# Kernel tuning notes

Measured on AMD Instinct MI355X. Metric: run time of the kernel, lower is better.

The kernel has to match this reference:

```python
import jax, jax.numpy as jnp
import numpy as np

N = 100000   # nodes
E = 1600000  # edges
DIN = 128
HID = 128
D2 = 64      # hard-coded last-conv width in the module
OUT = 1000


def setup_inputs() -> dict:
    key = jax.random.key(0)
    ks = jax.random.split(key, 8)
    x = jax.random.normal(ks[0], (N, DIN), dtype=jnp.float32)
    edge_index = jax.random.randint(ks[1], (2, E), 0, N, dtype=jnp.int64)
    W1 = jax.random.normal(ks[2], (DIN, HID), dtype=jnp.float32) * 0.05
    b1 = jnp.zeros((HID,), dtype=jnp.float32)
    W2 = jax.random.normal(ks[3], (HID, D2), dtype=jnp.float32) * 0.05
    b2 = jnp.zeros((D2,), dtype=jnp.float32)
    Wfc = jax.random.normal(ks[4], (D2, OUT), dtype=jnp.float32) * 0.05
    bfc = jnp.zeros((OUT,), dtype=jnp.float32)
    return {"x": x, "W1": W1, "b1": b1, "W2": W2, "b2": b2,
            "Wfc": Wfc, "bfc": bfc, "edge_index": edge_index}


def _gcn_conv(x, W, b, src, dst):
    # PyG GCNConv: h = X W; add self-loops; symmetric norm D^-1/2 (A+I) D^-1/2; + bias
    h = x @ W                                   # [N, F]
    ones = jnp.ones(src.shape[0], dtype=h.dtype)
    deg = jax.ops.segment_sum(ones, dst, num_segments=N) + 1.0  # +1 for self-loop
    dinv = jax.lax.rsqrt(deg)                   # [N]
    norm = dinv[src] * dinv[dst]                # [E]
    agg = jax.ops.segment_sum(h[src] * norm[:, None], dst, num_segments=N)
    agg = agg + h * (dinv * dinv)[:, None]      # self-loop contribution
    return agg + b


def reference(x, W1, b1, W2, b2, Wfc, bfc, edge_index):
    src, dst = edge_index[0], edge_index[1]
    h = jax.nn.relu(_gcn_conv(x, W1, b1, src, dst))
    # dropout is identity in eval mode (training=False)
    h = jax.nn.relu(_gcn_conv(h, W2, b2, src, dst))
    return h @ Wfc + bfc
```

## Files before the change

kernel.cpp:

```cpp
#include <hip/hip_runtime.h>
#include <hip/hip_bf16.h>
#include <cstddef>

typedef __attribute__((ext_vector_type(8))) short bf16x8;
typedef __attribute__((ext_vector_type(4))) float f32x4;

__device__ __forceinline__ unsigned short f2bf(float f) {
    __hip_bfloat16 h = __float2bfloat16(f);
    return __builtin_bit_cast(unsigned short, h);
}
__device__ __forceinline__ float bf2f(unsigned short u) {
    return __bfloat162float(__builtin_bit_cast(__hip_bfloat16, u));
}
__device__ __forceinline__ float bflo(unsigned u) {
    return __builtin_bit_cast(float, u << 16);
}
__device__ __forceinline__ float bfhi(unsigned u) {
    return __builtin_bit_cast(float, u & 0xffff0000u);
}


__global__ void k_zero_i(int* __restrict__ p, int total) {
    int i = blockIdx.x * blockDim.x + threadIdx.x;
    int stride = gridDim.x * blockDim.x;
    for (; i < total; i += stride) p[i] = 0;
}


__global__ void k_deg_i(const int* __restrict__ dst, int* __restrict__ deg, int E) {
    int e = blockIdx.x * blockDim.x + threadIdx.x;
    if (e < E) atomicAdd(&deg[dst[e]], 1);
}


#define SCAN_B 1024

__global__ void k_scan1(const int* __restrict__ in, int* __restrict__ out,
                        int* __restrict__ sums, float* __restrict__ dinv, int n) {
    __shared__ int tmp[SCAN_B];
    int tid = threadIdx.x;
    int gid = blockIdx.x * SCAN_B + tid;
    int v = (gid < n) ? in[gid] : 0;
    if (gid < n) dinv[gid] = rsqrtf((float)v + 1.0f);
    tmp[tid] = v;
    __syncthreads();
    for (int off = 1; off < SCAN_B; off <<= 1) {
        int t = (tid >= off) ? tmp[tid - off] : 0;
        __syncthreads();
        tmp[tid] += t;
        __syncthreads();
    }
    if (gid < n) out[gid] = tmp[tid] - v;
    if (tid == SCAN_B - 1) sums[blockIdx.x] = tmp[tid];
}

__global__ void k_scan2(int* __restrict__ sums, int nb) {
    __shared__ int tmp[128];
    int tid = threadIdx.x;
    int v = (tid < nb) ? sums[tid] : 0;
    tmp[tid] = v;
    __syncthreads();
    for (int off = 1; off < 128; off <<= 1) {
        int t = (tid >= off) ? tmp[tid - off] : 0;
        __syncthreads();
        tmp[tid] += t;
        __syncthreads();
    }
    if (tid < nb) sums[tid] = tmp[tid] - v;
}

__global__ void k_scan3(int* __restrict__ out, int* __restrict__ cursor,
                        const int* __restrict__ sums, int n) {
    int gid = blockIdx.x * SCAN_B + threadIdx.x;
    if (gid < n) {
        int v = out[gid] + sums[blockIdx.x];
        out[gid] = v;
        cursor[gid] = v;
    }
}


__global__ void k_fill(const int* __restrict__ src, const int* __restrict__ dst,
                       int* __restrict__ cursor, int* __restrict__ csr_src, int E) {
    int e = blockIdx.x * blockDim.x + threadIdx.x;
    if (e < E) {
        int pos = atomicAdd(&cursor[dst[e]], 1);
        csr_src[pos] = src[e];
    }
}


__global__ void k_conv_w_bf(const float* __restrict__ W, unsigned short* __restrict__ Bh,
                            int K, int N)
{
    int n = blockIdx.x;
    int k = threadIdx.x;
    Bh[(size_t)n * K + k] = f2bf(W[(size_t)k * N + n]);
}

__global__ void k_conv_w(const float* __restrict__ W, unsigned short* __restrict__ Bh,
                         unsigned short* __restrict__ Bl, int K, int N)
{
    int n = blockIdx.x;
    int k = threadIdx.x;
    float v = W[(size_t)k * N + n];
    unsigned short hi = f2bf(v);
    unsigned short lo = f2bf(v - bf2f(hi));
    Bh[(size_t)n * K + k] = hi;
    Bl[(size_t)n * K + k] = lo;
}


__device__ __forceinline__ void unpack_fma(float* a, float w, uint4 v) {
    a[0] = fmaf(w, bflo(v.x), a[0]);
    a[1] = fmaf(w, bfhi(v.x), a[1]);
    a[2] = fmaf(w, bflo(v.y), a[2]);
    a[3] = fmaf(w, bfhi(v.y), a[3]);
    a[4] = fmaf(w, bflo(v.z), a[4]);
    a[5] = fmaf(w, bfhi(v.z), a[5]);
    a[6] = fmaf(w, bflo(v.w), a[6]);
    a[7] = fmaf(w, bfhi(v.w), a[7]);
}

__launch_bounds__(256)
__global__ void k_gather128(const unsigned short* __restrict__ hbf,
                            const int* __restrict__ csr_src, const int* __restrict__ off,
                            const float* __restrict__ dinv, const float* __restrict__ bias,
                            unsigned short* __restrict__ obf, int N, int E)
{
    int node = blockIdx.x * 4 + (threadIdx.x >> 6);
    int lane = threadIdx.x & 63;
    if (node >= N) return;
    float dn = dinv[node];
    int beg = off[node];
    int end = (node + 1 < N) ? off[node + 1] : E;

    const int grp = lane >> 4;
    const int sub = lane & 15;

    uint4 sv = make_uint4(0, 0, 0, 0);
    float4 b0 = make_float4(0.f, 0.f, 0.f, 0.f), b1 = b0;
    if (grp == 0) {
        sv = *(const uint4*)(hbf + (size_t)node * 128 + sub * 8);
        b0 = *(const float4*)(bias + sub * 8);
        b1 = *(const float4*)(bias + sub * 8 + 4);
    }

    float a[8] = {0.f, 0.f, 0.f, 0.f, 0.f, 0.f, 0.f, 0.f};
    int i = beg + grp;
    for (; i + 12 < end; i += 16) {
        int s0 = csr_src[i];
        int s1 = csr_src[i + 4];
        int s2 = csr_src[i + 8];
        int s3 = csr_src[i + 12];
        float w0 = dinv[s0] * dn;
        float w1 = dinv[s1] * dn;
        float w2 = dinv[s2] * dn;
        float w3 = dinv[s3] * dn;
        uint4 v0 = *(const uint4*)(hbf + (size_t)s0 * 128 + sub * 8);
        uint4 v1 = *(const uint4*)(hbf + (size_t)s1 * 128 + sub * 8);
        uint4 v2 = *(const uint4*)(hbf + (size_t)s2 * 128 + sub * 8);
        uint4 v3 = *(const uint4*)(hbf + (size_t)s3 * 128 + sub * 8);
        unpack_fma(a, w0, v0);
        unpack_fma(a, w1, v1);
        unpack_fma(a, w2, v2);
        unpack_fma(a, w3, v3);
    }
    for (; i < end; i += 4) {
        int s = csr_src[i];
        float w = dinv[s] * dn;
        uint4 v = *(const uint4*)(hbf + (size_t)s * 128 + sub * 8);
        unpack_fma(a, w, v);
    }

#pragma unroll
    for (int k = 0; k < 8; ++k) {
        a[k] += __shfl_xor(a[k], 16);
        a[k] += __shfl_xor(a[k], 32);
    }

    if (grp == 0) {
        float s[8] = {bflo(sv.x), bfhi(sv.x), bflo(sv.y), bfhi(sv.y),
                      bflo(sv.z), bfhi(sv.z), bflo(sv.w), bfhi(sv.w)};
        float bv[8] = {b0.x, b0.y, b0.z, b0.w, b1.x, b1.y, b1.z, b1.w};
        float w = dn * dn;
        unsigned short o[8];
#pragma unroll
        for (int k = 0; k < 8; ++k)
            o[k] = f2bf(fmaxf(fmaf(s[k], w, a[k]) + bv[k], 0.f));
        uint4 vo;
        vo.x = (unsigned)o[0] | ((unsigned)o[1] << 16);
        vo.y = (unsigned)o[2] | ((unsigned)o[3] << 16);
        vo.z = (unsigned)o[4] | ((unsigned)o[5] << 16);
        vo.w = (unsigned)o[6] | ((unsigned)o[7] << 16);
        *(uint4*)(obf + (size_t)node * 128 + sub * 8) = vo;
    }
}


__launch_bounds__(256)
__global__ void k_gather64(const unsigned short* __restrict__ hbf,
                           const int* __restrict__ csr_src, const int* __restrict__ off,
                           const float* __restrict__ dinv, const float* __restrict__ bias,
                           unsigned short* __restrict__ hhi, unsigned short* __restrict__ hlo,
                           int N, int E)
{
    int node = blockIdx.x * 4 + (threadIdx.x >> 6);
    int lane = threadIdx.x & 63;
    if (node >= N) return;
    float dn = dinv[node];
    int beg = off[node];
    int end = (node + 1 < N) ? off[node + 1] : E;

    const int grp = lane >> 3;
    const int sub = lane & 7;

    uint4 sv = make_uint4(0, 0, 0, 0);
    float4 b0 = make_float4(0.f, 0.f, 0.f, 0.f), b1 = b0;
    if (grp == 0) {
        sv = *(const uint4*)(hbf + (size_t)node * 64 + sub * 8);
        b0 = *(const float4*)(bias + sub * 8);
        b1 = *(const float4*)(bias + sub * 8 + 4);
    }

    float a[8] = {0.f, 0.f, 0.f, 0.f, 0.f, 0.f, 0.f, 0.f};
    int i = beg + grp;
    for (; i + 8 < end; i += 16) {
        int s0 = csr_src[i];
        int s1 = csr_src[i + 8];
        float w0 = dinv[s0] * dn;
        float w1 = dinv[s1] * dn;
        uint4 v0 = *(const uint4*)(hbf + (size_t)s0 * 64 + sub * 8);
        uint4 v1 = *(const uint4*)(hbf + (size_t)s1 * 64 + sub * 8);
        unpack_fma(a, w0, v0);
        unpack_fma(a, w1, v1);
    }
    if (i < end) {
        int s = csr_src[i];
        float w = dinv[s] * dn;
        uint4 v = *(const uint4*)(hbf + (size_t)s * 64 + sub * 8);
        unpack_fma(a, w, v);
    }

#pragma unroll
    for (int k = 0; k < 8; ++k) {
        a[k] += __shfl_xor(a[k], 8);
        a[k] += __shfl_xor(a[k], 16);
        a[k] += __shfl_xor(a[k], 32);
    }

    if (grp == 0) {
        float s[8] = {bflo(sv.x), bfhi(sv.x), bflo(sv.y), bfhi(sv.y),
                      bflo(sv.z), bfhi(sv.z), bflo(sv.w), bfhi(sv.w)};
        float bv[8] = {b0.x, b0.y, b0.z, b0.w, b1.x, b1.y, b1.z, b1.w};
        float w = dn * dn;
        unsigned short hi[8], lo[8];
#pragma unroll
        for (int k = 0; k < 8; ++k) {
            float f = fmaxf(fmaf(s[k], w, a[k]) + bv[k], 0.f);
            hi[k] = f2bf(f);
            lo[k] = f2bf(f - bf2f(hi[k]));
        }
        uint4 vh, vl;
        vh.x = (unsigned)hi[0] | ((unsigned)hi[1] << 16);
        vh.y = (unsigned)hi[2] | ((unsigned)hi[3] << 16);
        vh.z = (unsigned)hi[4] | ((unsigned)hi[5] << 16);
        vh.w = (unsigned)hi[6] | ((unsigned)hi[7] << 16);
        vl.x = (unsigned)lo[0] | ((unsigned)lo[1] << 16);
        vl.y = (unsigned)lo[2] | ((unsigned)lo[3] << 16);
        vl.z = (unsigned)lo[4] | ((unsigned)lo[5] << 16);
        vl.w = (unsigned)lo[6] | ((unsigned)lo[7] << 16);
        *(uint4*)(hhi + (size_t)node * 64 + sub * 8) = vh;
        *(uint4*)(hlo + (size_t)node * 64 + sub * 8) = vl;
    }
}


__launch_bounds__(256, 2)
__global__ void gemm_mfma_l1(const float* __restrict__ A,
                             const unsigned short* __restrict__ Bt,
                             unsigned short* __restrict__ Cbf, int M)
{
    __shared__ unsigned short Ah[128 * 64];
    __shared__ unsigned short Bh[128 * 64];

    const int tid = threadIdx.x;
    const int m0 = blockIdx.x * 128;
    const int lane = tid & 63, wave = tid >> 6;
    const int wr = wave >> 1, wc = wave & 1;
    const int lrow = lane & 15, kgrp = lane >> 4;

    f32x4 acc[4][4] = {};

    for (int ph = 0; ph < 2; ++ph) {
        const int k0 = ph * 64;
        __syncthreads();
        {
            const int c4 = tid & 15, r0 = tid >> 4;
#pragma unroll
            for (int p = 0; p < 8; ++p) {
                int row = r0 + p * 16;
                int gr = m0 + row; if (gr >= M) gr = M - 1;
                float4 v = *(const float4*)(A + (size_t)gr * 128 + k0 + c4 * 4);
                ushort4 hv;
                hv.x = f2bf(v.x); hv.y = f2bf(v.y); hv.z = f2bf(v.z); hv.w = f2bf(v.w);
                *(ushort4*)((char*)Ah + row * 128 + ((c4 * 8) ^ ((row & 7) << 4))) = hv;
            }
        }
        {
            const int c = tid & 7, col0 = tid >> 3;
#pragma unroll
            for (int p = 0; p < 4; ++p) {
                int col = col0 + p * 32;
                uint4 v = *(const uint4*)(Bt + (size_t)col * 128 + k0 + c * 8);
                *(uint4*)((char*)Bh + col * 128 + ((c * 16) ^ ((col & 7) << 4))) = v;
            }
        }
        __syncthreads();

#pragma unroll
        for (int ks = 0; ks < 2; ++ks) {
            const int cIdx = kgrp + ks * 4;
            bf16x8 ah[4], bh[4];
#pragma unroll
            for (int i = 0; i < 4; ++i) {
                int row = wr * 64 + i * 16 + lrow;
                ah[i] = *(const bf16x8*)((const char*)Ah + row * 128 + ((cIdx * 16) ^ ((row & 7) << 4)));
            }
#pragma unroll
            for (int j = 0; j < 4; ++j) {
                int col = wc * 64 + j * 16 + lrow;
                bh[j] = *(const bf16x8*)((const char*)Bh + col * 128 + ((cIdx * 16) ^ ((col & 7) << 4)));
            }
#pragma unroll
            for (int i = 0; i < 4; ++i)
#pragma unroll
                for (int j = 0; j < 4; ++j)
                    acc[i][j] = __builtin_amdgcn_mfma_f32_16x16x32_bf16(bh[j], ah[i], acc[i][j], 0, 0, 0);
        }
    }

#pragma unroll
    for (int i = 0; i < 4; ++i) {
        int grow = m0 + wr * 64 + i * 16 + lrow;
        if (grow >= M) continue;
        unsigned short* crow = Cbf + (size_t)grow * 128;
#pragma unroll
        for (int j = 0; j < 4; ++j) {
            int gc = wc * 64 + j * 16 + kgrp * 4;
            ushort4 o;
            o.x = f2bf(acc[i][j][0]);
            o.y = f2bf(acc[i][j][1]);
            o.z = f2bf(acc[i][j][2]);
            o.w = f2bf(acc[i][j][3]);
            *(ushort4*)(crow + gc) = o;
        }
    }
}


__launch_bounds__(256, 3)
__global__ void gemm_mfma_l2(const unsigned short* __restrict__ Abf,
                             const unsigned short* __restrict__ Bt,
                             unsigned short* __restrict__ Cbf, int M)
{
    __shared__ unsigned short Ah[128 * 64];
    __shared__ unsigned short Bh[64 * 64];

    const int tid = threadIdx.x;
    const int m0 = blockIdx.x * 128;
    const int lane = tid & 63, wave = tid >> 6;
    const int wr = wave >> 1, wc = wave & 1;
    const int lrow = lane & 15, kgrp = lane >> 4;

    f32x4 acc[4][2] = {};

    for (int ph = 0; ph < 2; ++ph) {
        const int k0 = ph * 64;
        __syncthreads();
        {
            const int c = tid & 7, r0 = tid >> 3;
#pragma unroll
            for (int p = 0; p < 4; ++p) {
                int row = r0 + p * 32;
                int gr = m0 + row; if (gr >= M) gr = M - 1;
                uint4 v = *(const uint4*)(Abf + (size_t)gr * 128 + k0 + c * 8);
                *(uint4*)((char*)Ah + row * 128 + ((c * 16) ^ ((row & 7) << 4))) = v;
            }
        }
        {
            const int c = tid & 7, col0 = tid >> 3;
#pragma unroll
            for (int p = 0; p < 2; ++p) {
                int col = col0 + p * 32;
                uint4 v = *(const uint4*)(Bt + (size_t)col * 128 + k0 + c * 8);
                *(uint4*)((char*)Bh + col * 128 + ((c * 16) ^ ((col & 7) << 4))) = v;
            }
        }
        __syncthreads();

#pragma unroll
        for (int ks = 0; ks < 2; ++ks) {
            const int cIdx = kgrp + ks * 4;
            bf16x8 ah[4], bh[2];
#pragma unroll
            for (int i = 0; i < 4; ++i) {
                int row = wr * 64 + i * 16 + lrow;
                ah[i] = *(const bf16x8*)((const char*)Ah + row * 128 + ((cIdx * 16) ^ ((row & 7) << 4)));
            }
#pragma unroll
            for (int j = 0; j < 2; ++j) {
                int col = wc * 32 + j * 16 + lrow;
                bh[j] = *(const bf16x8*)((const char*)Bh + col * 128 + ((cIdx * 16) ^ ((col & 7) << 4)));
            }
#pragma unroll
            for (int i = 0; i < 4; ++i)
#pragma unroll
                for (int j = 0; j < 2; ++j)
                    acc[i][j] = __builtin_amdgcn_mfma_f32_16x16x32_bf16(bh[j], ah[i], acc[i][j], 0, 0, 0);
        }
    }

#pragma unroll
    for (int i = 0; i < 4; ++i) {
        int grow = m0 + wr * 64 + i * 16 + lrow;
        if (grow >= M) continue;
        unsigned short* crow = Cbf + (size_t)grow * 64;
#pragma unroll
        for (int j = 0; j < 2; ++j) {
            int gc = wc * 32 + j * 16 + kgrp * 4;
            ushort4 o;
            o.x = f2bf(acc[i][j][0]);
            o.y = f2bf(acc[i][j][1]);
            o.z = f2bf(acc[i][j][2]);
            o.w = f2bf(acc[i][j][3]);
            *(ushort4*)(crow + gc) = o;
        }
    }
}


__launch_bounds__(256, 3)
__global__ void gemm_mfma_out(const unsigned short* __restrict__ Ahi,
                              const unsigned short* __restrict__ Alo,
                              const unsigned short* __restrict__ Bhi,
                              const unsigned short* __restrict__ Blo,
                              const float* __restrict__ bias, float* __restrict__ C,
                              int M, int N)
{
    const int tid = threadIdx.x;
    const int lane = tid & 63, wave = tid >> 6;
    const int wr = wave >> 1, wc = wave & 1;
    const int m0 = blockIdx.y * 128 + wr * 64;
    const int n0 = blockIdx.x * 128 + wc * 64;
    const int lrow = lane & 15, kgrp = lane >> 4;

    f32x4 acc[4][4] = {};

#pragma unroll
    for (int ks = 0; ks < 2; ++ks) {
        const int koff = (kgrp + ks * 4) * 8;
        bf16x8 ah[4], al[4], bh[4], bl[4];
#pragma unroll
        for (int i = 0; i < 4; ++i) {
            int row = m0 + i * 16 + lrow; if (row >= M) row = M - 1;
            ah[i] = *(const bf16x8*)(Ahi + (size_t)row * 64 + koff);
            al[i] = *(const bf16x8*)(Alo + (size_t)row * 64 + koff);
        }
#pragma unroll
        for (int j = 0; j < 4; ++j) {
            int col = n0 + j * 16 + lrow; if (col >= N) col = N - 1;
            bh[j] = *(const bf16x8*)(Bhi + (size_t)col * 64 + koff);
            bl[j] = *(const bf16x8*)(Blo + (size_t)col * 64 + koff);
        }
#pragma unroll
        for (int i = 0; i < 4; ++i)
#pragma unroll
            for (int j = 0; j < 4; ++j) {
                acc[i][j] = __builtin_amdgcn_mfma_f32_16x16x32_bf16(bh[j], ah[i], acc[i][j], 0, 0, 0);
                acc[i][j] = __builtin_amdgcn_mfma_f32_16x16x32_bf16(bl[j], ah[i], acc[i][j], 0, 0, 0);
                acc[i][j] = __builtin_amdgcn_mfma_f32_16x16x32_bf16(bh[j], al[i], acc[i][j], 0, 0, 0);
            }
    }

#pragma unroll
    for (int i = 0; i < 4; ++i) {
        int grow = m0 + i * 16 + lrow;
        if (grow >= M) continue;
        float* crow = C + (size_t)grow * N;
#pragma unroll
        for (int j = 0; j < 4; ++j) {
            int gc = n0 + j * 16 + kgrp * 4;
            if (gc + 4 <= N) {
                float4 bv = *(const float4*)(bias + gc);
                *(float4*)(crow + gc) = make_float4(acc[i][j][0] + bv.x,
                                                    acc[i][j][1] + bv.y,
                                                    acc[i][j][2] + bv.z,
                                                    acc[i][j][3] + bv.w);
            }
        }
    }
}


extern "C" void kernel_launch(void* const* d_in, const int* in_sizes, int n_in,
                              void* d_out, int out_size, void* d_ws, size_t ws_size,
                              hipStream_t stream)
{
    const float* x   = (const float*)d_in[0];
    const float* W1  = (const float*)d_in[1];
    const float* b1  = (const float*)d_in[2];
    const float* W2  = (const float*)d_in[3];
    const float* b2  = (const float*)d_in[4];
    const float* Wfc = (const float*)d_in[5];
    const float* bfc = (const float*)d_in[6];
    const int*   ei  = (const int*)d_in[7];

    const int Nn = in_sizes[0] / 128;
    const int E  = in_sizes[7] / 2;
    const int* src = ei;
    const int* dst = ei + E;

    char* ws = (char*)d_ws;
    float*          dinv   = (float*)(ws);
    unsigned short* Wfc_hi = (unsigned short*)(ws + 512 * 1024);
    unsigned short* Wfc_lo = (unsigned short*)(ws + 768 * 1024);
    unsigned short* W1_bf  = (unsigned short*)(ws + 1024 * 1024);
    unsigned short* W2_bf  = (unsigned short*)(ws + 1088 * 1024);
    unsigned short* h2hi   = (unsigned short*)(ws + 1152 * 1024);
    unsigned short* h2lo   = (unsigned short*)(ws + 1152 * 1024 + (size_t)Nn * 64 * 2);

    char* ob = (char*)d_out;
    unsigned short* hbf     = (unsigned short*)ob;
    unsigned short* h1bf    = (unsigned short*)(ob + (size_t)Nn * 256);
    unsigned short* h2bf    = (unsigned short*)(ob + (size_t)Nn * 512);
    int*            csr_src = (int*)(ob + (size_t)Nn * 640);
    int*            offs    = (int*)((char*)csr_src + (size_t)E * 4);
    int*            cursor  = (int*)((char*)offs + (size_t)Nn * 4);
    int*            deg_cnt = (int*)((char*)cursor + (size_t)Nn * 4);
    int*            bsums   = (int*)((char*)deg_cnt + (size_t)Nn * 4);

    const int nScanBlocks = (Nn + SCAN_B - 1) / SCAN_B;

    k_zero_i<<<128, 256, 0, stream>>>(deg_cnt, Nn);
    k_deg_i<<<(E + 255) / 256, 256, 0, stream>>>(dst, deg_cnt, E);
    k_scan1<<<nScanBlocks, SCAN_B, 0, stream>>>(deg_cnt, offs, bsums, dinv, Nn);
    k_scan2<<<1, 128, 0, stream>>>(bsums, nScanBlocks);
    k_scan3<<<nScanBlocks, SCAN_B, 0, stream>>>(offs, cursor, bsums, Nn);
    k_fill<<<(E + 255) / 256, 256, 0, stream>>>(src, dst, cursor, csr_src, E);
    k_conv_w_bf<<<128, 128, 0, stream>>>(W1, W1_bf, 128, 128);
    k_conv_w_bf<<<64, 128, 0, stream>>>(W2, W2_bf, 128, 64);
    k_conv_w<<<1000, 64, 0, stream>>>(Wfc, Wfc_hi, Wfc_lo, 64, 1000);

    gemm_mfma_l1<<<dim3((Nn + 127) / 128, 1), 256, 0, stream>>>(x, W1_bf, hbf, Nn);
    k_gather128<<<(Nn + 3) / 4, 256, 0, stream>>>(hbf, csr_src, offs, dinv, b1,
                                                  h1bf, Nn, E);

    gemm_mfma_l2<<<dim3((Nn + 127) / 128, 1), 256, 0, stream>>>(h1bf, W2_bf, h2bf, Nn);
    k_gather64<<<(Nn + 3) / 4, 256, 0, stream>>>(h2bf, csr_src, offs, dinv, b2,
                                                 h2hi, h2lo, Nn, E);

    gemm_mfma_out<<<dim3((1000 + 127) / 128, (Nn + 127) / 128), 256, 0, stream>>>(
        h2hi, h2lo, Wfc_hi, Wfc_lo, bfc, (float*)d_out, Nn, 1000);
}
```

Baseline: 523.9 us.

## Stage Wfc tiles in swizzled LDS and merge weight-conversion launches

The output GEMM now loads its 128-column hi/lo weight tile once into XOR-swizzled shared memory. Each block then processes two 128-row M tiles against it, halving the block count and the repeated global weight loads. The three small weight-conversion kernels are merged into one launch to cut launch overhead. The cost is 32 KB of LDS per block, which may lower occupancy, plus an extra barrier before compute.

```diff
diff --git a/kernel.cpp b/kernel.cpp
--- a/kernel.cpp
+++ b/kernel.cpp
@@ -90,24 +90,27 @@
 }
 
 
-__global__ void k_conv_w_bf(const float* __restrict__ W, unsigned short* __restrict__ Bh,
-                            int K, int N)
-{
-    int n = blockIdx.x;
+__global__ void k_conv_all(const float* __restrict__ W1, const float* __restrict__ W2,
+                           const float* __restrict__ Wfc,
+                           unsigned short* __restrict__ W1bf, unsigned short* __restrict__ W2bf,
+                           unsigned short* __restrict__ Wfch, unsigned short* __restrict__ Wfcl)
+{
+    int b = blockIdx.x;
     int k = threadIdx.x;
-    Bh[(size_t)n * K + k] = f2bf(W[(size_t)k * N + n]);
-}
-
-__global__ void k_conv_w(const float* __restrict__ W, unsigned short* __restrict__ Bh,
-                         unsigned short* __restrict__ Bl, int K, int N)
-{
-    int n = blockIdx.x;
-    int k = threadIdx.x;
-    float v = W[(size_t)k * N + n];
-    unsigned short hi = f2bf(v);
-    unsigned short lo = f2bf(v - bf2f(hi));
-    Bh[(size_t)n * K + k] = hi;
-    Bl[(size_t)n * K + k] = lo;
+    if (b < 128) {
+        W1bf[(size_t)b * 128 + k] = f2bf(W1[(size_t)k * 128 + b]);
+    } else if (b < 192) {
+        int n = b - 128;
+        W2bf[(size_t)n * 128 + k] = f2bf(W2[(size_t)k * 64 + n]);
+    } else {
+        int n = b - 192;
+        if (k < 64) {
+            float v = Wfc[(size_t)k * 1000 + n];
+            unsigned short hi = f2bf(v);
+            Wfch[(size_t)n * 64 + k] = hi;
+            Wfcl[(size_t)n * 64 + k] = f2bf(v - bf2f(hi));
+        }
+    }
 }
 
 
@@ -448,55 +451,79 @@
                               const float* __restrict__ bias, float* __restrict__ C,
                               int M, int N)
 {
+    __shared__ unsigned short Bh[128 * 64], Bl[128 * 64];
+
     const int tid = threadIdx.x;
+    const int nbase = blockIdx.x * 128;
+
+    {
+        const int c = tid & 7, col0 = tid >> 3;
+#pragma unroll
+        for (int p = 0; p < 4; ++p) {
+            int col = col0 + p * 32;
+            int gcol = nbase + col; if (gcol >= N) gcol = N - 1;
+            uint4 v = *(const uint4*)(Bhi + (size_t)gcol * 64 + c * 8);
+            uint4 w = *(const uint4*)(Blo + (size_t)gcol * 64 + c * 8);
+            int off = col * 128 + ((c * 16) ^ ((col & 7) << 4));
+            *(uint4*)((char*)Bh + off) = v;
+            *(uint4*)((char*)Bl + off) = w;
+        }
+    }
+    __syncthreads();
+
     const int lane = tid & 63, wave = tid >> 6;
     const int wr = wave >> 1, wc = wave & 1;
-    const int m0 = blockIdx.y * 128 + wr * 64;
-    const int n0 = blockIdx.x * 128 + wc * 64;
     const int lrow = lane & 15, kgrp = lane >> 4;
-
-    f32x4 acc[4][4] = {};
-
-#pragma unroll
-    for (int ks = 0; ks < 2; ++ks) {
-        const int koff = (kgrp + ks * 4) * 8;
-        bf16x8 ah[4], al[4], bh[4], bl[4];
+    const int n0 = nbase + wc * 64;
+
+#pragma unroll
+    for (int mt = 0; mt < 2; ++mt) {
+        const int m0 = (blockIdx.y * 2 + mt) * 128 + wr * 64;
+        f32x4 acc[4][4] = {};
+
+#pragma unroll
+        for (int ks = 0; ks < 2; ++ks) {
+            const int cIdx = kgrp + ks * 4;
+            const int koff = cIdx * 8;
+            bf16x8 ah[4], al[4], bh[4], bl[4];
+#pragma unroll
+            for (int i = 0; i < 4; ++i) {
+                int row = m0 + i * 16 + lrow; if (row >= M) row = M - 1;
+                ah[i] = *(const bf16x8*)(Ahi + (size_t)row * 64 + koff);
+                al[i] = *(const bf16x8*)(Alo + (size_t)row * 64 + koff);
+            }
+#pragma unroll
+            for (int j = 0; j < 4; ++j) {
+                int col = wc * 64 + j * 16 + lrow;
+                int off = col * 128 + ((cIdx * 16) ^ ((col & 7) << 4));
+                bh[j] = *(const bf16x8*)((const char*)Bh + off);
+                bl[j] = *(const bf16x8*)((const char*)Bl + off);
+            }
+#pragma unroll
+            for (int i = 0; i < 4; ++i)
+#pragma unroll
+                for (int j = 0; j < 4; ++j) {
+                    acc[i][j] = __builtin_amdgcn_mfma_f32_16x16x32_bf16(bh[j], ah[i], acc[i][j], 0, 0, 0);
+                    acc[i][j] = __builtin_amdgcn_mfma_f32_16x16x32_bf16(bl[j], ah[i], acc[i][j], 0, 0, 0);
+                    acc[i][j] = __builtin_amdgcn_mfma_f32_16x16x32_bf16(bh[j], al[i], acc[i][j], 0, 0, 0);
+                }
+        }
+
 #pragma unroll
         for (int i = 0; i < 4; ++i) {
-            int row = m0 + i * 16 + lrow; if (row >= M) row = M - 1;
-            ah[i] = *(const bf16x8*)(Ahi + (size_t)row * 64 + koff);
-            al[i] = *(const bf16x8*)(Alo + (size_t)row * 64 + koff);
-        }
-#pragma unroll
-        for (int j = 0; j < 4; ++j) {
-            int col = n0 + j * 16 + lrow; if (col >= N) col = N - 1;
-            bh[j] = *(const bf16x8*)(Bhi + (size_t)col * 64 + koff);
-            bl[j] = *(const bf16x8*)(Blo + (size_t)col * 64 + koff);
-        }
-#pragma unroll
-        for (int i = 0; i < 4; ++i)
+            int grow = m0 + i * 16 + lrow;
+            if (grow >= M) continue;
+            float* crow = C + (size_t)grow * N;
 #pragma unroll
             for (int j = 0; j < 4; ++j) {
-                acc[i][j] = __builtin_amdgcn_mfma_f32_16x16x32_bf16(bh[j], ah[i], acc[i][j], 0, 0, 0);
-                acc[i][j] = __builtin_amdgcn_mfma_f32_16x16x32_bf16(bl[j], ah[i], acc[i][j], 0, 0, 0);
-                acc[i][j] = __builtin_amdgcn_mfma_f32_16x16x32_bf16(bh[j], al[i], acc[i][j], 0, 0, 0);
-            }
-    }
-
-#pragma unroll
-    for (int i = 0; i < 4; ++i) {
-        int grow = m0 + i * 16 + lrow;
-        if (grow >= M) continue;
-        float* crow = C + (size_t)grow * N;
-#pragma unroll
-        for (int j = 0; j < 4; ++j) {
-            int gc = n0 + j * 16 + kgrp * 4;
-            if (gc + 4 <= N) {
-                float4 bv = *(const float4*)(bias + gc);
-                *(float4*)(crow + gc) = make_float4(acc[i][j][0] + bv.x,
-                                                    acc[i][j][1] + bv.y,
-                                                    acc[i][j][2] + bv.z,
-                                                    acc[i][j][3] + bv.w);
+                int gc = n0 + j * 16 + kgrp * 4;
+                if (gc + 4 <= N) {
+                    float4 bv = *(const float4*)(bias + gc);
+                    *(float4*)(crow + gc) = make_float4(acc[i][j][0] + bv.x,
+                                                        acc[i][j][1] + bv.y,
+                                                        acc[i][j][2] + bv.z,
+                                                        acc[i][j][3] + bv.w);
+                }
             }
         }
     }
@@ -548,9 +575,7 @@
     k_scan2<<<1, 128, 0, stream>>>(bsums, nScanBlocks);
     k_scan3<<<nScanBlocks, SCAN_B, 0, stream>>>(offs, cursor, bsums, Nn);
     k_fill<<<(E + 255) / 256, 256, 0, stream>>>(src, dst, cursor, csr_src, E);
-    k_conv_w_bf<<<128, 128, 0, stream>>>(W1, W1_bf, 128, 128);
-    k_conv_w_bf<<<64, 128, 0, stream>>>(W2, W2_bf, 128, 64);
-    k_conv_w<<<1000, 64, 0, stream>>>(Wfc, Wfc_hi, Wfc_lo, 64, 1000);
+    k_conv_all<<<1192, 128, 0, stream>>>(W1, W2, Wfc, W1_bf, W2_bf, Wfc_hi, Wfc_lo);
 
     gemm_mfma_l1<<<dim3((Nn + 127) / 128, 1), 256, 0, stream>>>(x, W1_bf, hbf, Nn);
     k_gather128<<<(Nn + 3) / 4, 256, 0, stream>>>(hbf, csr_src, offs, dinv, b1,
@@ -560,6 +585,6 @@
     k_gather64<<<(Nn + 3) / 4, 256, 0, stream>>>(h2bf, csr_src, offs, dinv, b2,
                                                  h2hi, h2lo, Nn, E);
 
-    gemm_mfma_out<<<dim3((1000 + 127) / 128, (Nn + 127) / 128), 256, 0, stream>>>(
+    gemm_mfma_out<<<dim3(8, (Nn + 255) / 256), 256, 0, stream>>>(
         h2hi, h2lo, Wfc_hi, Wfc_lo, bfc, (float*)d_out, Nn, 1000);
 }
```

Measured after the change: 505.5 us, median of 3. -3.5%, faster.
